# Optimization experiments

Hardware: AMD Instinct MI355X
Metric: run time of the kernel (lower is better)

## Reference

```python
import jax, jax.numpy as jnp
import numpy as np


def setup_inputs() -> dict:
    key = jax.random.key(0)
    k1, k2, k3, k4, k5 = jax.random.split(key, 5)
    NNZ = 1_600_000
    N, IN, OUT = 8192, 4096, 4096
    vals = jax.random.normal(k1, (NNZ,), dtype=jnp.float32)
    rows = jax.random.randint(k2, (NNZ,), 0, N, dtype=jnp.int32)
    cols = jax.random.randint(k3, (NNZ,), 0, IN, dtype=jnp.int32)
    # kaiming_uniform-ish init scale for weight, uniform bias
    bound_w = jnp.sqrt(1.0 / IN)
    weight = jax.random.uniform(k4, (OUT, IN), dtype=jnp.float32, minval=-bound_w, maxval=bound_w)
    bias = jax.random.uniform(k5, (OUT,), dtype=jnp.float32, minval=-bound_w, maxval=bound_w)
    return {"vals": vals, "rows": rows, "cols": cols, "weight": weight, "bias": bias, "n_rows": N}


def reference(vals, rows, cols, weight, bias, n_rows):
    """Sparse COO [n_rows, in_features] @ weight.T + bias (torch.sparse.addmm).

    Densify via scatter-add (COO semantics: duplicate indices accumulate),
    then a single dense GEMM which dominates the cost.
    """
    in_features = weight.shape[1]
    dense = jnp.zeros((n_rows, in_features), dtype=vals.dtype).at[rows, cols].add(vals)
    return dense @ weight.T + bias  # [n_rows, out_features]
```

## Files before the change

kernel.cpp:

```cpp
#include <hip/hip_runtime.h>

typedef __attribute__((ext_vector_type(8)))  __bf16 bf16x8;
typedef __attribute__((ext_vector_type(4)))  float  f32x4;
typedef __attribute__((ext_vector_type(8)))  unsigned short u16x8;

__device__ inline unsigned short f2bf(float f) {
    unsigned int u = __float_as_uint(f);
    u += 0x7FFFu + ((u >> 16) & 1u);
    return (unsigned short)(u >> 16);
}

__global__ __launch_bounds__(256) void scatter_cvt(
        const float* __restrict__ vals,
        const int* __restrict__ rows,
        const int* __restrict__ cols,
        unsigned short* __restrict__ Ab,
        int nnz, int in_f,
        const float* __restrict__ wsrc,
        unsigned short* __restrict__ wdst,
        long nW, int cvtBlocks) {
    if ((int)blockIdx.x < cvtBlocks) {
        long i = ((long)blockIdx.x * 256 + threadIdx.x) * 8;
        if (i + 8 <= nW) {
            f32x4 a = *(const f32x4*)(wsrc + i);
            f32x4 b = *(const f32x4*)(wsrc + i + 4);
            u16x8 o;
            o[0] = f2bf(a[0]); o[1] = f2bf(a[1]); o[2] = f2bf(a[2]); o[3] = f2bf(a[3]);
            o[4] = f2bf(b[0]); o[5] = f2bf(b[1]); o[6] = f2bf(b[2]); o[7] = f2bf(b[3]);
            *(u16x8*)(wdst + i) = o;
        }
        return;
    }
    int i = ((int)blockIdx.x - cvtBlocks) * 256 + threadIdx.x;
    if (i >= nnz) return;
    float v = vals[i];
    size_t idx = (size_t)rows[i] * in_f + cols[i];
#if __has_builtin(__builtin_amdgcn_global_atomic_fadd_v2bf16)
    typedef __attribute__((ext_vector_type(2))) short s16x2;
    unsigned short hv = f2bf(v);
    s16x2 add;
    add[0] = (idx & 1) ? (short)0 : (short)hv;
    add[1] = (idx & 1) ? (short)hv : (short)0;
    __builtin_amdgcn_global_atomic_fadd_v2bf16(
        (__attribute__((address_space(1))) s16x2*)(Ab + (idx & ~(size_t)1)), add);
#else
    unsigned int* word = (unsigned int*)(Ab + (idx & ~(size_t)1));
    unsigned int sh = (unsigned int)(idx & 1) * 16u;
    unsigned int old = *word, assumed;
    do {
        assumed = old;
        unsigned int cur = (assumed >> sh) & 0xFFFFu;
        float f = __uint_as_float(cur << 16) + v;
        unsigned int nb = f2bf(f);
        unsigned int repl = (assumed & ~(0xFFFFu << sh)) | (nb << sh);
        old = atomicCAS(word, assumed, repl);
    } while (old != assumed);
#endif
}


__device__ __forceinline__ bf16x8 read_frag(const unsigned short* hb, int rowl, int c) {
    int cs = c ^ (rowl & 7);
    return *(const bf16x8*)(hb + rowl * 64 + (cs << 3));
}

__device__ __forceinline__ void stage_half(const unsigned short* __restrict__ G,
                                           int grow0, int K, int kbase,
                                           unsigned short* hb, int tid) {
    const int lane = tid & 63, wv = tid >> 6;
    #pragma unroll
    for (int j = 0; j < 2; ++j) {
        int u = j * 512 + wv * 64 + lane;
        int rowl = u >> 3;
        int c = (u & 7) ^ (rowl & 7);
        const unsigned short* g = G + (size_t)(grow0 + rowl) * K + kbase + c * 8;
        unsigned short* l = hb + (size_t)(j * 512 + wv * 64) * 8;
        __builtin_amdgcn_global_load_lds(
            (const __attribute__((address_space(1))) void*)g,
            (__attribute__((address_space(3))) void*)l, 16, 0, 0);
    }
}

__global__ __launch_bounds__(512, 2) void gemm_bt_bias(
    const unsigned short* __restrict__ A,
    const unsigned short* __restrict__ B,
    const float* __restrict__ bias,
    float* __restrict__ C,
    int M, int N, int K)
{
    __shared__ unsigned short sA[2][2][8192];
    __shared__ unsigned short sB[2][2][8192];

    const int tid  = threadIdx.x;
    const int lane = tid & 63;
    const int wave = tid >> 6;
    const int wm = (wave >> 2) * 128;
    const int wn = (wave & 3) * 64;
    const int r15 = lane & 15;
    const int g   = lane >> 4;
    const int ah  = wm >> 7;
    const int bh  = wn >> 7;
    const int bro = wn & 64;

    const int nbx = gridDim.x;
    const int nwg = gridDim.x * gridDim.y;
    int flat = blockIdx.y * gridDim.x + blockIdx.x;
    int rid = (nwg & 7) ? flat : ((flat & 7) * (nwg >> 3) + (flat >> 3));
    const int bm = (rid / nbx) * 256;
    const int bn = (rid % nbx) * 256;

    f32x4 acc[8][4];
    #pragma unroll
    for (int i = 0; i < 8; ++i)
        #pragma unroll
        for (int jg = 0; jg < 4; ++jg)
            #pragma unroll
            for (int r = 0; r < 4; ++r) acc[i][jg][r] = 0.f;

    stage_half(A, bm,       K, 0,  &sA[0][0][0], tid);
    stage_half(A, bm + 128, K, 0,  &sA[0][1][0], tid);
    stage_half(B, bn,       K, 0,  &sB[0][0][0], tid);
    stage_half(B, bn + 128, K, 0,  &sB[0][1][0], tid);
    stage_half(A, bm,       K, 64, &sA[1][0][0], tid);
    stage_half(A, bm + 128, K, 64, &sA[1][1][0], tid);
    asm volatile("s_waitcnt vmcnt(4)" ::: "memory");
    __builtin_amdgcn_s_barrier();

    const int nt = K >> 6;
    for (int t = 0; t < nt; ++t) {
        const int cur = t & 1, nxt = cur ^ 1;
        const int t1k = ((t + 1 < nt) ? t + 1 : 0) << 6;
        const int t2k = ((t + 2 < nt) ? t + 2 : 0) << 6;
        const unsigned short* sAh = &sA[cur][ah][0];
        const unsigned short* sBh = &sB[cur][bh][0];

        bf16x8 a[8], b0, b1;

        #pragma unroll
        for (int i = 0; i < 8; ++i) a[i] = read_frag(sAh, i * 16 + r15, g);
        b0 = read_frag(sBh, bro + r15, g);
        b1 = read_frag(sBh, bro + 16 + r15, g);
        stage_half(B, bn,       K, t1k, &sB[nxt][0][0], tid);
        stage_half(B, bn + 128, K, t1k, &sB[nxt][1][0], tid);
        __builtin_amdgcn_s_barrier();
        asm volatile("s_waitcnt lgkmcnt(0)" ::: "memory");
        __builtin_amdgcn_sched_barrier(0);
        __builtin_amdgcn_s_setprio(1);
        #pragma unroll
        for (int i = 0; i < 8; ++i) {
            acc[i][0] = __builtin_amdgcn_mfma_f32_16x16x32_bf16(a[i], b0, acc[i][0], 0, 0, 0);
            acc[i][1] = __builtin_amdgcn_mfma_f32_16x16x32_bf16(a[i], b1, acc[i][1], 0, 0, 0);
        }
        __builtin_amdgcn_s_setprio(0);
        __builtin_amdgcn_s_barrier();

        b0 = read_frag(sBh, bro + 32 + r15, g);
        b1 = read_frag(sBh, bro + 48 + r15, g);
        __builtin_amdgcn_s_barrier();
        asm volatile("s_waitcnt lgkmcnt(0)" ::: "memory");
        __builtin_amdgcn_sched_barrier(0);
        __builtin_amdgcn_s_setprio(1);
        #pragma unroll
        for (int i = 0; i < 8; ++i) {
            acc[i][2] = __builtin_amdgcn_mfma_f32_16x16x32_bf16(a[i], b0, acc[i][2], 0, 0, 0);
            acc[i][3] = __builtin_amdgcn_mfma_f32_16x16x32_bf16(a[i], b1, acc[i][3], 0, 0, 0);
        }
        __builtin_amdgcn_s_setprio(0);
        __builtin_amdgcn_s_barrier();

        #pragma unroll
        for (int i = 0; i < 8; ++i) a[i] = read_frag(sAh, i * 16 + r15, 4 + g);
        b0 = read_frag(sBh, bro + r15, 4 + g);
        b1 = read_frag(sBh, bro + 16 + r15, 4 + g);
        __builtin_amdgcn_s_barrier();
        asm volatile("s_waitcnt lgkmcnt(0)" ::: "memory");
        __builtin_amdgcn_sched_barrier(0);
        __builtin_amdgcn_s_setprio(1);
        #pragma unroll
        for (int i = 0; i < 8; ++i) {
            acc[i][0] = __builtin_amdgcn_mfma_f32_16x16x32_bf16(a[i], b0, acc[i][0], 0, 0, 0);
            acc[i][1] = __builtin_amdgcn_mfma_f32_16x16x32_bf16(a[i], b1, acc[i][1], 0, 0, 0);
        }
        __builtin_amdgcn_s_setprio(0);
        __builtin_amdgcn_s_barrier();

        b0 = read_frag(sBh, bro + 32 + r15, 4 + g);
        b1 = read_frag(sBh, bro + 48 + r15, 4 + g);
        stage_half(A, bm,       K, t2k, &sA[cur][0][0], tid);
        stage_half(A, bm + 128, K, t2k, &sA[cur][1][0], tid);
        __builtin_amdgcn_s_barrier();
        asm volatile("s_waitcnt lgkmcnt(0)" ::: "memory");
        __builtin_amdgcn_sched_barrier(0);
        __builtin_amdgcn_s_setprio(1);
        #pragma unroll
        for (int i = 0; i < 8; ++i) {
            acc[i][2] = __builtin_amdgcn_mfma_f32_16x16x32_bf16(a[i], b0, acc[i][2], 0, 0, 0);
            acc[i][3] = __builtin_amdgcn_mfma_f32_16x16x32_bf16(a[i], b1, acc[i][3], 0, 0, 0);
        }
        __builtin_amdgcn_s_setprio(0);
        asm volatile("s_waitcnt vmcnt(4)" ::: "memory");
        __builtin_amdgcn_s_barrier();
    }
    asm volatile("s_waitcnt vmcnt(0)" ::: "memory");

    #pragma unroll
    for (int jg = 0; jg < 4; ++jg) {
        int col = bn + wn + jg * 16 + r15;
        float bv = bias[col];
        #pragma unroll
        for (int i = 0; i < 8; ++i) {
            int rbase = bm + wm + i * 16 + g * 4;
            #pragma unroll
            for (int r = 0; r < 4; ++r) {
                __builtin_nontemporal_store(acc[i][jg][r] + bv,
                                            &C[(size_t)(rbase + r) * N + col]);
            }
        }
    }
}

extern "C" void kernel_launch(void* const* d_in, const int* in_sizes, int n_in,
                              void* d_out, int out_size, void* d_ws, size_t ws_size,
                              hipStream_t stream) {
    const float* vals   = (const float*)d_in[0];
    const int*   rows   = (const int*)d_in[1];
    const int*   cols   = (const int*)d_in[2];
    const float* weight = (const float*)d_in[3];
    const float* bias   = (const float*)d_in[4];

    const int NNZ = in_sizes[0];
    const int OUT = in_sizes[4];
    const int IN  = in_sizes[3] / OUT;
    const int M   = out_size / OUT;

    unsigned short* Ab = (unsigned short*)d_ws;
    size_t abBytes = (size_t)M * IN * sizeof(unsigned short);
    unsigned short* Wb = (unsigned short*)((char*)d_ws + abBytes);

    hipMemsetAsync(Ab, 0, abBytes, stream);

    {
        long nW = (long)OUT * IN;
        int cvtBlocks = (int)((nW / 8 + 255) / 256);
        int scBlocks  = (NNZ + 255) / 256;
        scatter_cvt<<<cvtBlocks + scBlocks, 256, 0, stream>>>(
            vals, rows, cols, Ab, NNZ, IN, weight, Wb, nW, cvtBlocks);
    }

    dim3 grid(OUT / 256, M / 256);
    gemm_bt_bias<<<grid, 512, 0, stream>>>(Ab, Wb, bias, (float*)d_out, M, OUT, IN);
}
```

Measured before the change: 513.4 us.

## Switch GEMM to 32x32x16 MFMA with fewer barriers per K-tile

Replaces the 16x16x32 MFMA tiles with 32x32x16 bf16 MFMAs, so each wave holds a 4x2 grid of 32x32 accumulators and reads fewer LDS fragments per FLOP. The K-tile pipeline is also restructured: A and B are both double-buffered two tiles ahead and refilled together after a single wait-and-barrier point, replacing the four barrier-separated phases of the old loop. This is meant to cut LDS read traffic and synchronisation overhead. The trade-off is a full vmcnt(0) wait every iteration, which may expose global-load latency, and an LDS read pattern whose bank conflicts have changed.

```diff
diff --git a/kernel.cpp b/kernel.cpp
--- a/kernel.cpp
+++ b/kernel.cpp
@@ -1,6 +1,7 @@
 #include <hip/hip_runtime.h>
 
 typedef __attribute__((ext_vector_type(8)))  __bf16 bf16x8;
+typedef __attribute__((ext_vector_type(16))) float  f32x16;
 typedef __attribute__((ext_vector_type(4)))  float  f32x4;
 typedef __attribute__((ext_vector_type(8)))  unsigned short u16x8;
 
@@ -59,8 +60,8 @@
 }
 
 
-__device__ __forceinline__ bf16x8 read_frag(const unsigned short* hb, int rowl, int c) {
-    int cs = c ^ (rowl & 7);
+__device__ __forceinline__ bf16x8 read_frag(const unsigned short* hb, int rowl, int slot) {
+    int cs = slot ^ (rowl & 7);
     return *(const bf16x8*)(hb + rowl * 64 + (cs << 3));
 }
 
@@ -96,8 +97,8 @@
     const int wave = tid >> 6;
     const int wm = (wave >> 2) * 128;
     const int wn = (wave & 3) * 64;
-    const int r15 = lane & 15;
-    const int g   = lane >> 4;
+    const int m32 = lane & 31;
+    const int h   = lane >> 5;
     const int ah  = wm >> 7;
     const int bh  = wn >> 7;
     const int bro = wn & 64;
@@ -109,13 +110,13 @@
     const int bm = (rid / nbx) * 256;
     const int bn = (rid % nbx) * 256;
 
-    f32x4 acc[8][4];
+    f32x16 acc[4][2];
     #pragma unroll
-    for (int i = 0; i < 8; ++i)
+    for (int i = 0; i < 4; ++i)
         #pragma unroll
-        for (int jg = 0; jg < 4; ++jg)
-            #pragma unroll
-            for (int r = 0; r < 4; ++r) acc[i][jg][r] = 0.f;
+        for (int j = 0; j < 2; ++j)
+            #pragma unroll
+            for (int r = 0; r < 16; ++r) acc[i][j][r] = 0.f;
 
     stage_half(A, bm,       K, 0,  &sA[0][0][0], tid);
     stage_half(A, bm + 128, K, 0,  &sA[0][1][0], tid);
@@ -123,97 +124,95 @@
     stage_half(B, bn + 128, K, 0,  &sB[0][1][0], tid);
     stage_half(A, bm,       K, 64, &sA[1][0][0], tid);
     stage_half(A, bm + 128, K, 64, &sA[1][1][0], tid);
-    asm volatile("s_waitcnt vmcnt(4)" ::: "memory");
+    stage_half(B, bn,       K, 64, &sB[1][0][0], tid);
+    stage_half(B, bn + 128, K, 64, &sB[1][1][0], tid);
+    asm volatile("s_waitcnt vmcnt(8)" ::: "memory");
     __builtin_amdgcn_s_barrier();
 
     const int nt = K >> 6;
     for (int t = 0; t < nt; ++t) {
-        const int cur = t & 1, nxt = cur ^ 1;
-        const int t1k = ((t + 1 < nt) ? t + 1 : 0) << 6;
+        const int cur = t & 1;
         const int t2k = ((t + 2 < nt) ? t + 2 : 0) << 6;
         const unsigned short* sAh = &sA[cur][ah][0];
         const unsigned short* sBh = &sB[cur][bh][0];
 
-        bf16x8 a[8], b0, b1;
-
-        #pragma unroll
-        for (int i = 0; i < 8; ++i) a[i] = read_frag(sAh, i * 16 + r15, g);
-        b0 = read_frag(sBh, bro + r15, g);
-        b1 = read_frag(sBh, bro + 16 + r15, g);
-        stage_half(B, bn,       K, t1k, &sB[nxt][0][0], tid);
-        stage_half(B, bn + 128, K, t1k, &sB[nxt][1][0], tid);
-        __builtin_amdgcn_s_barrier();
-        asm volatile("s_waitcnt lgkmcnt(0)" ::: "memory");
-        __builtin_amdgcn_sched_barrier(0);
-        __builtin_amdgcn_s_setprio(1);
-        #pragma unroll
-        for (int i = 0; i < 8; ++i) {
-            acc[i][0] = __builtin_amdgcn_mfma_f32_16x16x32_bf16(a[i], b0, acc[i][0], 0, 0, 0);
-            acc[i][1] = __builtin_amdgcn_mfma_f32_16x16x32_bf16(a[i], b1, acc[i][1], 0, 0, 0);
-        }
-        __builtin_amdgcn_s_setprio(0);
-        __builtin_amdgcn_s_barrier();
-
-        b0 = read_frag(sBh, bro + 32 + r15, g);
-        b1 = read_frag(sBh, bro + 48 + r15, g);
-        __builtin_amdgcn_s_barrier();
-        asm volatile("s_waitcnt lgkmcnt(0)" ::: "memory");
-        __builtin_amdgcn_sched_barrier(0);
-        __builtin_amdgcn_s_setprio(1);
-        #pragma unroll
-        for (int i = 0; i < 8; ++i) {
-            acc[i][2] = __builtin_amdgcn_mfma_f32_16x16x32_bf16(a[i], b0, acc[i][2], 0, 0, 0);
-            acc[i][3] = __builtin_amdgcn_mfma_f32_16x16x32_bf16(a[i], b1, acc[i][3], 0, 0, 0);
-        }
-        __builtin_amdgcn_s_setprio(0);
-        __builtin_amdgcn_s_barrier();
-
-        #pragma unroll
-        for (int i = 0; i < 8; ++i) a[i] = read_frag(sAh, i * 16 + r15, 4 + g);
-        b0 = read_frag(sBh, bro + r15, 4 + g);
-        b1 = read_frag(sBh, bro + 16 + r15, 4 + g);
-        __builtin_amdgcn_s_barrier();
-        asm volatile("s_waitcnt lgkmcnt(0)" ::: "memory");
-        __builtin_amdgcn_sched_barrier(0);
-        __builtin_amdgcn_s_setprio(1);
-        #pragma unroll
-        for (int i = 0; i < 8; ++i) {
-            acc[i][0] = __builtin_amdgcn_mfma_f32_16x16x32_bf16(a[i], b0, acc[i][0], 0, 0, 0);
-            acc[i][1] = __builtin_amdgcn_mfma_f32_16x16x32_bf16(a[i], b1, acc[i][1], 0, 0, 0);
-        }
-        __builtin_amdgcn_s_setprio(0);
-        __builtin_amdgcn_s_barrier();
-
-        b0 = read_frag(sBh, bro + 32 + r15, 4 + g);
-        b1 = read_frag(sBh, bro + 48 + r15, 4 + g);
-        stage_half(A, bm,       K, t2k, &sA[cur][0][0], tid);
-        stage_half(A, bm + 128, K, t2k, &sA[cur][1][0], tid);
-        __builtin_amdgcn_s_barrier();
-        asm volatile("s_waitcnt lgkmcnt(0)" ::: "memory");
-        __builtin_amdgcn_sched_barrier(0);
-        __builtin_amdgcn_s_setprio(1);
-        #pragma unroll
-        for (int i = 0; i < 8; ++i) {
-            acc[i][2] = __builtin_amdgcn_mfma_f32_16x16x32_bf16(a[i], b0, acc[i][2], 0, 0, 0);
-            acc[i][3] = __builtin_amdgcn_mfma_f32_16x16x32_bf16(a[i], b1, acc[i][3], 0, 0, 0);
-        }
-        __builtin_amdgcn_s_setprio(0);
-        asm volatile("s_waitcnt vmcnt(4)" ::: "memory");
-        __builtin_amdgcn_s_barrier();
+        {
+            bf16x8 a0[4], a1[4], b0[2], b1[2];
+            #pragma unroll
+            for (int i = 0; i < 4; ++i) {
+                int rl = i * 32 + m32;
+                a0[i] = read_frag(sAh, rl, h);
+                a1[i] = read_frag(sAh, rl, 2 + h);
+            }
+            #pragma unroll
+            for (int j = 0; j < 2; ++j) {
+                int rl = bro + j * 32 + m32;
+                b0[j] = read_frag(sBh, rl, h);
+                b1[j] = read_frag(sBh, rl, 2 + h);
+            }
+            __builtin_amdgcn_s_setprio(1);
+            #pragma unroll
+            for (int i = 0; i < 4; ++i)
+                #pragma unroll
+                for (int j = 0; j < 2; ++j)
+                    acc[i][j] = __builtin_amdgcn_mfma_f32_32x32x16_bf16(a0[i], b0[j], acc[i][j], 0, 0, 0);
+            #pragma unroll
+            for (int i = 0; i < 4; ++i)
+                #pragma unroll
+                for (int j = 0; j < 2; ++j)
+                    acc[i][j] = __builtin_amdgcn_mfma_f32_32x32x16_bf16(a1[i], b1[j], acc[i][j], 0, 0, 0);
+            __builtin_amdgcn_s_setprio(0);
+        }
+
+        {
+            bf16x8 a0[4], a1[4], b0[2], b1[2];
+            #pragma unroll
+            for (int i = 0; i < 4; ++i) {
+                int rl = i * 32 + m32;
+                a0[i] = read_frag(sAh, rl, 4 + h);
+                a1[i] = read_frag(sAh, rl, 6 + h);
+            }
+            #pragma unroll
+            for (int j = 0; j < 2; ++j) {
+                int rl = bro + j * 32 + m32;
+                b0[j] = read_frag(sBh, rl, 4 + h);
+                b1[j] = read_frag(sBh, rl, 6 + h);
+            }
+            asm volatile("s_waitcnt vmcnt(0) lgkmcnt(0)" ::: "memory");
+            __builtin_amdgcn_sched_barrier(0);
+            __builtin_amdgcn_s_barrier();
+            stage_half(A, bm,       K, t2k, &sA[cur][0][0], tid);
+            stage_half(A, bm + 128, K, t2k, &sA[cur][1][0], tid);
+            stage_half(B, bn,       K, t2k, &sB[cur][0][0], tid);
+            stage_half(B, bn + 128, K, t2k, &sB[cur][1][0], tid);
+            __builtin_amdgcn_s_setprio(1);
+            #pragma unroll
+            for (int i = 0; i < 4; ++i)
+                #pragma unroll
+                for (int j = 0; j < 2; ++j)
+                    acc[i][j] = __builtin_amdgcn_mfma_f32_32x32x16_bf16(a0[i], b0[j], acc[i][j], 0, 0, 0);
+            #pragma unroll
+            for (int i = 0; i < 4; ++i)
+                #pragma unroll
+                for (int j = 0; j < 2; ++j)
+                    acc[i][j] = __builtin_amdgcn_mfma_f32_32x32x16_bf16(a1[i], b1[j], acc[i][j], 0, 0, 0);
+            __builtin_amdgcn_s_setprio(0);
+        }
     }
     asm volatile("s_waitcnt vmcnt(0)" ::: "memory");
 
     #pragma unroll
-    for (int jg = 0; jg < 4; ++jg) {
-        int col = bn + wn + jg * 16 + r15;
+    for (int j = 0; j < 2; ++j) {
+        int col = bn + wn + j * 32 + m32;
         float bv = bias[col];
         #pragma unroll
-        for (int i = 0; i < 8; ++i) {
-            int rbase = bm + wm + i * 16 + g * 4;
-            #pragma unroll
-            for (int r = 0; r < 4; ++r) {
-                __builtin_nontemporal_store(acc[i][jg][r] + bv,
-                                            &C[(size_t)(rbase + r) * N + col]);
+        for (int i = 0; i < 4; ++i) {
+            int rbase = bm + wm + i * 32 + 4 * h;
+            #pragma unroll
+            for (int r = 0; r < 16; ++r) {
+                int row = rbase + (r & 3) + 8 * (r >> 2);
+                __builtin_nontemporal_store(acc[i][j][r] + bv,
+                                            &C[(size_t)row * N + col]);
             }
         }
     }
```

Result: faster. 487.5 us (-5.0%).
